# Kernel tuning notes

Hardware: AMD Instinct MI355X
Metric: run time of the kernel (lower is better)

Reference implementation:

```python
import jax, jax.numpy as jnp
import numpy as np

NB, BS = 64, 128          # num_blocks, block_size (W.shape[1]=8192)
TAU = 3.0                 # iteration=0 -> start temperature
SINKHORN_ITERS = 5


def sinkhorn(logits, tau=TAU, iters=SINKHORN_ITERS):
    P = jax.nn.softmax(logits / tau, axis=-1)
    for _ in range(iters):
        P = P / P.sum(axis=-1, keepdims=True)
        P = P / P.sum(axis=-2, keepdims=True)
    return P


def _lsa_min(cost):
    """Hungarian (Jonker-Volgenant / e-maxx) min-cost assignment on a square
    matrix; returns col index for each row. Matches scipy.linear_sum_assignment."""
    cost = np.asarray(cost, np.float64)
    n = cost.shape[0]
    INF = 1e18
    u = np.zeros(n + 1)
    v = np.zeros(n + 1)
    p = np.zeros(n + 1, np.int64)  # p[j] = row (1-based) assigned to column j
    for i in range(1, n + 1):
        p[0] = i
        j0 = 0
        minv = np.full(n + 1, INF)
        used = np.zeros(n + 1, bool)
        way = np.zeros(n + 1, np.int64)
        while True:
            used[j0] = True
            i0 = p[j0]
            free = ~used[1:]
            cur = cost[i0 - 1] - u[i0] - v[1:]
            upd = free & (cur < minv[1:])
            minv[1:][upd] = cur[upd]
            way[1:][upd] = j0
            masked = np.where(free, minv[1:], INF)
            j1 = int(np.argmin(masked)) + 1
            delta = masked[j1 - 1]
            u[p[used]] += delta
            v[used] -= delta
            minv[1:][free] -= delta
            j0 = j1
            if p[j0] == 0:
                break
        while j0 != 0:  # augment along alternating path
            j1 = way[j0]
            p[j0] = p[j1]
            j0 = j1
    col_of_row = np.empty(n, np.int64)
    col_of_row[p[1:] - 1] = np.arange(n)
    return col_of_row


def hungarian_hard(P_np):
    """Per-block hard permutation maximizing P (i.e. min cost = -P)."""
    nb, bs, _ = P_np.shape
    hard = np.zeros((nb, bs, bs), np.float32)
    rows = np.arange(bs)
    for b in range(nb):
        hard[b, rows, _lsa_min(-P_np[b])] = 1.0
    return hard


def _soft_perm(weight, scale):
    w = weight * scale
    # torch: weight.data.clamp_(-1, 1)  -> straight-through clamp
    w = w + jax.lax.stop_gradient(jnp.clip(w, -1.0, 1.0) - w)
    return sinkhorn(w)


def _assemble(blocks):
    nb, bs, _ = blocks.shape
    G = nb * bs
    idx = jnp.arange(nb)
    out = jnp.zeros((nb, bs, nb, bs), blocks.dtype)
    out = out.at[idx, :, idx, :].set(blocks)
    return out.reshape(G, G)


def setup_inputs() -> dict:
    key = jax.random.key(0)
    k1, _ = jax.random.split(key)
    bound = 1.0 / np.sqrt(BS)
    weight = jax.random.uniform(k1, (NB, BS, BS), jnp.float32, -bound, bound)
    scale = jnp.asarray(np.sqrt(BS), jnp.float32)
    return {"weight": weight, "scale": scale}


def reference(weight, scale):
    P = _soft_perm(weight, scale)                       # (NB, BS, BS)
    hard = jnp.asarray(hungarian_hard(np.asarray(P)))   # constant hard perms
    # STE: (hard - P).detach() + P  ==  hard + (P - stop_grad(P))
    blocks = hard + (P - jax.lax.stop_gradient(P))
    return _assemble(blocks)                             # (8192, 8192)
```

## Files before the change

kernel.cpp:

```cpp
#include <hip/hip_runtime.h>
#include <hip/hip_bf16.h>

#define NBLK 64
#define BS   128
#define GSZ  8192

__device__ __forceinline__ int rl32(int v, int sl) {
    return __builtin_amdgcn_readlane(v, sl);
}
__device__ __forceinline__ double rl64(double v, int sl) {
    union { double d; unsigned u[2]; } a; a.d = v;
    unsigned lo = (unsigned)__builtin_amdgcn_readlane((int)a.u[0], sl);
    unsigned hi = (unsigned)__builtin_amdgcn_readlane((int)a.u[1], sl);
    union { unsigned u[2]; double d; } r; r.u[0] = lo; r.u[1] = hi;
    return r.d;
}
__device__ __forceinline__ unsigned long long pkey16(double m, int pj, int col) {
    union { double d; unsigned long long u; } a; a.d = m;
    unsigned long long x = a.u;
    x = (x >> 63) ? ~x : (x | 0x8000000000000000ull);
    return (x & ~0xFFFFull) | ((unsigned long long)(unsigned)pj << 8)
                            | (unsigned long long)(unsigned)col;
}
__device__ __forceinline__ double key16_val(unsigned long long k) {
    unsigned long long x = k & ~0xFFFFull;
    x = (x & 0x8000000000000000ull) ? (x & 0x7FFFFFFFFFFFFFFFull) : ~x;
    union { unsigned long long u; double d; } r; r.u = x;
    return r.d;
}

__device__ __forceinline__ unsigned long long wave_min_key64(unsigned long long k) {
    unsigned lo = (unsigned)k, hi = (unsigned)(k >> 32);
#define WMK_STEP(ctrl, rmask)                                                           \
    {                                                                                   \
        unsigned nlo = (unsigned)__builtin_amdgcn_update_dpp((int)lo, (int)lo, ctrl, rmask, 0xf, false); \
        unsigned nhi = (unsigned)__builtin_amdgcn_update_dpp((int)hi, (int)hi, ctrl, rmask, 0xf, false); \
        unsigned long long ny  = ((unsigned long long)nhi << 32) | nlo;                 \
        unsigned long long cur = ((unsigned long long)hi  << 32) | lo;                  \
        if (ny < cur) { lo = nlo; hi = nhi; }                                           \
    }
    WMK_STEP(0x111, 0xf)
    WMK_STEP(0x112, 0xf)
    WMK_STEP(0x114, 0xf)
    WMK_STEP(0x118, 0xf)
    WMK_STEP(0x142, 0xa)
    WMK_STEP(0x143, 0xc)
#undef WMK_STEP
    unsigned mlo = (unsigned)__builtin_amdgcn_readlane((int)lo, 63);
    unsigned mhi = (unsigned)__builtin_amdgcn_readlane((int)hi, 63);
    return ((unsigned long long)mhi << 32) | mlo;
}

__global__ __launch_bounds__(256) void k_fused(const float* __restrict__ w,
                                               const float* __restrict__ scale_p,
                                               float* __restrict__ out) {
    __shared__ float M[BS][BS + 1];
    __shared__ int   rowasg[BS];
    float* Mf = &M[0][0];

    const int b = blockIdx.x;
    const int t = threadIdx.x;
    const float scale = *scale_p;

    if (t < BS) {
        for (int r = 0; r < BS; ++r) {
            float x = w[((size_t)b * BS + r) * BS + t] * scale;
            x = fminf(fmaxf(x, -1.0f), 1.0f);
            M[r][t] = x / 3.0f;
        }
    }
    __syncthreads();
    if (t < BS) {
        float mx = M[t][0];
        for (int c = 1; c < BS; ++c) mx = fmaxf(mx, M[t][c]);
        float s = 0.0f;
        for (int c = 0; c < BS; ++c) { float e = expf(M[t][c] - mx); M[t][c] = e; s += e; }
        float rs = 1.0f / s;
        for (int c = 0; c < BS; ++c) M[t][c] *= rs;
    }
    __syncthreads();
    for (int it = 0; it < 5; ++it) {
        if (t < BS) {
            float s = 0.0f;
            for (int c = 0; c < BS; ++c) s += M[t][c];
            float rs = 1.0f / s;
            for (int c = 0; c < BS; ++c) M[t][c] *= rs;
        }
        __syncthreads();
        if (t < BS) {
            float s = 0.0f;
            for (int r = 0; r < BS; ++r) s += M[r][t];
            float rs = 1.0f / s;
            for (int r = 0; r < BS; ++r) M[r][t] *= rs;
        }
        __syncthreads();
    }

    int pA = 0, pB = 0;

    if (t >= 64) {
        const int l = t - 64;
        float4 z = make_float4(0.f, 0.f, 0.f, 0.f);
        float4* o4 = reinterpret_cast<float4*>(out + (size_t)b * BS * GSZ);
        for (int k = l; k < BS * GSZ / 4; k += 192) o4[k] = z;
    } else {
        const int jAcol = t + 1, jBcol = t + 65;
        double uA = 0.0, uB = 0.0, vA, vB;

        {
            float cmA = Mf[t];      int raA = 0;
            float cmB = Mf[t + 64]; int raB = 0;
            for (int r = 1; r < BS; ++r) {
                float xA = Mf[r * (BS + 1) + t];
                if (xA > cmA) { cmA = xA; raA = r; }
                float xB = Mf[r * (BS + 1) + t + 64];
                if (xB > cmB) { cmB = xB; raB = r; }
            }
            vA = -(double)cmA; vB = -(double)cmB;
            rowasg[t] = 0x7FFFFFFF; rowasg[t + 64] = 0x7FFFFFFF;
            __threadfence_block();
            atomicMin(&rowasg[raA], jAcol);
            atomicMin(&rowasg[raB], jBcol);
            __threadfence_block();
            pA = (rowasg[raA] == jAcol) ? raA + 1 : 0;
            pB = (rowasg[raB] == jBcol) ? raB + 1 : 0;
        }

        unsigned long long un0 = __ballot(rowasg[t]      == 0x7FFFFFFF);
        unsigned long long un1 = __ballot(rowasg[t + 64] == 0x7FFFFFFF);

        for (int steps = 0; (un0 | un1) && steps < 512; ++steps) {
            int i;
            if (un0) i = __builtin_ctzll(un0) + 1;
            else     i = __builtin_ctzll(un1) + 65;

            double dA = -(double)Mf[(i - 1) * (BS + 1) + t]      - vA;
            double dB = -(double)Mf[(i - 1) * (BS + 1) + t + 64] - vB;
            unsigned long long kA = pkey16(dA, pA, jAcol), kB = pkey16(dB, pB, jBcol);

            unsigned long long k1 = wave_min_key64(kA < kB ? kA : kB);
            const int  j1  = (int)(k1 & 0xFFull);
            const int  i1  = (int)((k1 >> 8) & 0xFFull);
            const int  sl1 = (j1 - 1) & 63;
            const bool h1  = j1 > 64;
            double u1 = key16_val(k1);

            unsigned long long kA2 = (jAcol == j1) ? ~0ull : kA;
            unsigned long long kB2 = (jBcol == j1) ? ~0ull : kB;
            unsigned long long k2 = wave_min_key64(kA2 < kB2 ? kA2 : kB2);
            double u2 = key16_val(k2);

            if (t == sl1) {
                if (h1) { pB = i; uB = u2; if (u1 < u2) vB -= (u2 - u1); }
                else    { pA = i; uA = u2; if (u1 < u2) vA -= (u2 - u1); }
            }
            if (i <= 64) un0 &= ~(1ull << (i - 1)); else un1 &= ~(1ull << (i - 65));
            if (i1 > 0) {
                if (i1 <= 64) un0 |= 1ull << (i1 - 1); else un1 |= 1ull << (i1 - 65);
            }
        }

        while (un0 | un1) {
            int i;
            if (un0) { int r = __builtin_ctzll(un0); un0 &= un0 - 1; i = r + 1; }
            else     { int r = __builtin_ctzll(un1); un1 &= un1 - 1; i = r + 65; }

            bool usedA = false, usedB = false;
            unsigned long long keyA = ~0ull, keyB = ~0ull;
            int wayA = 0, wayB = 0;
            int i0 = i, j0 = 0;
            double ui0 = 0.0, SUM = 0.0;

            for (int guard = 0; guard <= BS + 2; ++guard) {
                float cAv = Mf[(i0 - 1) * (BS + 1) + t];
                float cBv = Mf[(i0 - 1) * (BS + 1) + t + 64];
                double baseA = SUM - ui0 - vA;
                double baseB = SUM - ui0 - vB;
                if (!usedA) {
                    unsigned long long nk = pkey16(baseA - (double)cAv, pA, jAcol);
                    if (nk < keyA) { keyA = nk; wayA = j0; }
                }
                if (!usedB) {
                    unsigned long long nk = pkey16(baseB - (double)cBv, pB, jBcol);
                    if (nk < keyB) { keyB = nk; wayB = j0; }
                }
                unsigned long long kw = wave_min_key64(keyA < keyB ? keyA : keyB);
                if (kw == ~0ull) break;
                const int  j1 = (int)(kw & 0xFFull);
                const int  pj = (int)((kw >> 8) & 0xFFull);
                const int  sl = (j1 - 1) & 63;
                const bool hb = j1 > 64;

                double m_win = key16_val(kw);
                double delta = m_win - SUM;
                SUM = m_win;
                if (usedA) { uA += delta; vA -= delta; }
                if (usedB) { uB += delta; vB -= delta; }

                j0 = j1;
                if (pj == 0) break;
                ui0 = rl64(hb ? uB : uA, sl);
                i0 = pj;
                if (t == sl) { if (hb) { usedB = true; keyB = ~0ull; }
                               else    { usedA = true; keyA = ~0ull; } }
            }

            int jc = j0;
            for (int guard = 0; guard <= BS + 2; ++guard) {
                const int  slc = (jc - 1) & 63;
                const bool hc  = jc > 64;
                int jp = rl32(hc ? wayB : wayA, slc);
                int nprow; double nu;
                if (jp == 0) { nprow = i; nu = SUM; }
                else {
                    const int  slp = (jp - 1) & 63;
                    const bool hp  = jp > 64;
                    nprow = rl32(hp ? pB : pA, slp);
                    nu    = rl64(hp ? uB : uA, slp);
                }
                if (!hc) { if (t == slc) { pA = nprow; uA = nu; } }
                else     { if (t == slc) { pB = nprow; uB = nu; } }
                if (jp == 0) break;
                jc = jp;
            }
        }
    }

    __syncthreads();

    if (t < 64) {
        const size_t base = (size_t)b * BS;
        if (pA >= 1) out[(base + (size_t)(pA - 1)) * GSZ + base + t]      = 1.0f;
        if (pB >= 1) out[(base + (size_t)(pB - 1)) * GSZ + base + t + 64] = 1.0f;
    }
}

extern "C" void kernel_launch(void* const* d_in, const int* in_sizes, int n_in,
                              void* d_out, int out_size, void* d_ws, size_t ws_size,
                              hipStream_t stream) {
    const float* w     = (const float*)d_in[0];
    const float* scale = (const float*)d_in[1];
    float* out = (float*)d_out;
    k_fused<<<NBLK, 256, 0, stream>>>(w, scale, out);
}
```

Before: 715.4 us.

## Add column-potential boost and second auction-style reduction pass before augmentation

After the first capped augmenting-row-reduction pass, recompute column potentials v from the current row potentials (stored in shared memory) and run a second guarded reduction pass that stops once the free-row count stops shrinking. It boosts v once more before the full shortest-augmenting-path phase. The aim is to leave fewer free rows for the expensive sequential Dijkstra-style augmentation, at the cost of extra O(BS^2) scans and a new shared array.

Result: slower. 783.5 us (+9.5%).

```diff
diff --git a/kernel.cpp b/kernel.cpp
--- a/kernel.cpp
+++ b/kernel.cpp
@@ -54,8 +54,9 @@
 __global__ __launch_bounds__(256) void k_fused(const float* __restrict__ w,
                                                const float* __restrict__ scale_p,
                                                float* __restrict__ out) {
-    __shared__ float M[BS][BS + 1];
-    __shared__ int   rowasg[BS];
+    __shared__ float  M[BS][BS + 1];
+    __shared__ int    rowasg[BS];
+    __shared__ double urowS[BS];
     float* Mf = &M[0][0];
 
     const int b = blockIdx.x;
@@ -129,36 +130,66 @@
         unsigned long long un0 = __ballot(rowasg[t]      == 0x7FFFFFFF);
         unsigned long long un1 = __ballot(rowasg[t + 64] == 0x7FFFFFFF);
 
-        for (int steps = 0; (un0 | un1) && steps < 512; ++steps) {
-            int i;
-            if (un0) i = __builtin_ctzll(un0) + 1;
-            else     i = __builtin_ctzll(un1) + 65;
-
-            double dA = -(double)Mf[(i - 1) * (BS + 1) + t]      - vA;
-            double dB = -(double)Mf[(i - 1) * (BS + 1) + t + 64] - vB;
-            unsigned long long kA = pkey16(dA, pA, jAcol), kB = pkey16(dB, pB, jBcol);
-
-            unsigned long long k1 = wave_min_key64(kA < kB ? kA : kB);
-            const int  j1  = (int)(k1 & 0xFFull);
-            const int  i1  = (int)((k1 >> 8) & 0xFFull);
-            const int  sl1 = (j1 - 1) & 63;
-            const bool h1  = j1 > 64;
-            double u1 = key16_val(k1);
-
-            unsigned long long kA2 = (jAcol == j1) ? ~0ull : kA;
-            unsigned long long kB2 = (jBcol == j1) ? ~0ull : kB;
-            unsigned long long k2 = wave_min_key64(kA2 < kB2 ? kA2 : kB2);
-            double u2 = key16_val(k2);
-
-            if (t == sl1) {
-                if (h1) { pB = i; uB = u2; if (u1 < u2) vB -= (u2 - u1); }
-                else    { pA = i; uA = u2; if (u1 < u2) vA -= (u2 - u1); }
-            }
-            if (i <= 64) un0 &= ~(1ull << (i - 1)); else un1 &= ~(1ull << (i - 65));
-            if (i1 > 0) {
-                if (i1 <= 64) un0 |= 1ull << (i1 - 1); else un1 |= 1ull << (i1 - 65);
-            }
-        }
+        volatile double* urow = urowS;
+        auto vboost = [&]() {
+            urow[t] = 0.0; urow[t + 64] = 0.0;
+            if (pA > 0) urow[pA - 1] = uA;
+            if (pB > 0) urow[pB - 1] = uB;
+            double mnA = 1e18, mnB = 1e18;
+            for (int r = 0; r < BS; ++r) {
+                double ur = urow[r];
+                mnA = fmin(mnA, -(double)Mf[r * (BS + 1) + t]      - ur);
+                mnB = fmin(mnB, -(double)Mf[r * (BS + 1) + t + 64] - ur);
+            }
+            if (pA == 0) vA = mnA;
+            if (pB == 0) vB = mnB;
+        };
+
+        auto arr_pass = [&](int cap, bool guarded) {
+            int lastFree = 2 * BS;
+            for (int steps = 0; (un0 | un1) && steps < cap; ++steps) {
+                int i;
+                if (un0) i = __builtin_ctzll(un0) + 1;
+                else     i = __builtin_ctzll(un1) + 65;
+
+                double dA = -(double)Mf[(i - 1) * (BS + 1) + t]      - vA;
+                double dB = -(double)Mf[(i - 1) * (BS + 1) + t + 64] - vB;
+                unsigned long long kA = pkey16(dA, pA, jAcol), kB = pkey16(dB, pB, jBcol);
+
+                unsigned long long k1 = wave_min_key64(kA < kB ? kA : kB);
+                const int  j1  = (int)(k1 & 0xFFull);
+                const int  i1  = (int)((k1 >> 8) & 0xFFull);
+                const int  sl1 = (j1 - 1) & 63;
+                const bool h1  = j1 > 64;
+                double u1 = key16_val(k1);
+
+                unsigned long long kA2 = (jAcol == j1) ? ~0ull : kA;
+                unsigned long long kB2 = (jBcol == j1) ? ~0ull : kB;
+                unsigned long long k2 = wave_min_key64(kA2 < kB2 ? kA2 : kB2);
+                double u2 = key16_val(k2);
+
+                if (t == sl1) {
+                    if (h1) { pB = i; uB = u2; if (u1 < u2) vB -= (u2 - u1); }
+                    else    { pA = i; uA = u2; if (u1 < u2) vA -= (u2 - u1); }
+                }
+                if (i <= 64) un0 &= ~(1ull << (i - 1)); else un1 &= ~(1ull << (i - 65));
+                if (i1 > 0) {
+                    if (i1 <= 64) un0 |= 1ull << (i1 - 1); else un1 |= 1ull << (i1 - 65);
+                }
+                if (guarded && (steps & 63) == 63) {
+                    int f = __popcll(un0) + __popcll(un1);
+                    if (f >= lastFree) break;
+                    lastFree = f;
+                }
+            }
+        };
+
+        arr_pass(512, false);
+        if (un0 | un1) {
+            vboost();
+            arr_pass(512, true);
+        }
+        if (un0 | un1) vboost();
 
         while (un0 | un1) {
             int i;
```
